# Optimization experiments

Measured on AMD Instinct MI355X. Metric: run time of the kernel, lower is better.

## Reference

```python
import jax, jax.numpy as jnp
import numpy as np


def setup_inputs() -> dict:
    key = jax.random.key(0)
    k1, k2 = jax.random.split(key)
    B, C, N = 8, 3, 4096
    ori_pcs = jax.random.normal(k1, (B, C, N), dtype=jnp.float32)
    adv_pcs = jax.random.normal(k2, (B, C, N), dtype=jnp.float32)
    return {"ori_pcs": ori_pcs, "adv_pcs": adv_pcs}


def _chamfer(ori_pcs, adv_pcs, single=False, reduce="max"):
    # [B, 3, N] -> [B, N, 3]
    x = jnp.swapaxes(ori_pcs, 1, 2)
    y = jnp.swapaxes(adv_pcs, 1, 2)
    x2 = jnp.sum(x * x, axis=-1)  # [B, N]
    y2 = jnp.sum(y * y, axis=-1)  # [B, M]
    # squared pairwise distances [B, N, M]
    d = x2[:, :, None] + y2[:, None, :] - 2.0 * jnp.einsum("bnd,bmd->bnm", x, y)
    d = jnp.maximum(d, 0.0)
    d1 = jnp.mean(jnp.min(d, axis=2), axis=1)  # ori -> adv, per batch [B]
    if single:
        return jnp.mean(d1)
    d2 = jnp.mean(jnp.min(d, axis=1), axis=1)  # adv -> ori, per batch [B]
    if reduce == "max":
        per_batch = jnp.maximum(d1, d2)
    else:  # 'sum' / 'mean' style fallback
        per_batch = d1 + d2
    return jnp.mean(per_batch)


def reference(ori_pcs, adv_pcs):
    return _chamfer(ori_pcs, adv_pcs, single=False, reduce="max")
```

## Files before the change

### kernel.cpp

```cpp
#include <hip/hip_runtime.h>
#include <float.h>

#define BATCH 8
#define NPTS 4096
#define BLK 256
#define THALF 1024
#define NH 4

typedef __attribute__((ext_vector_type(8))) short short8;
typedef __attribute__((ext_vector_type(16))) float floatx16;

union U4S8 { uint4 u; short8 s; };

__device__ inline unsigned short f2bf(float f) {
    unsigned u = __float_as_uint(f);
    return (unsigned short)((u + 0x7FFFu + ((u >> 16) & 1u)) >> 16);
}
__device__ inline float bf2f(unsigned short h) {
    return __uint_as_float(((unsigned)h) << 16);
}
__device__ inline unsigned flag_token(int i) {
    return 0x9E3779B9u * (unsigned)(i + 7);
}

__global__ __launch_bounds__(BLK, 4) void chamfer_partial(
        const float* __restrict__ ori, const float* __restrict__ adv,
        float* __restrict__ rfin) {
    __shared__ uint4 sm[THALF];

    int bx = blockIdx.x;
    int half = bx & (NH - 1);
    int rowgroup = (bx >> 2) & 15;
    int dirb = bx >> 6;
    int b = dirb & 7;
    int dir = dirb >> 3;

    const float* qsrc = dir ? adv : ori;
    const float* tsrc = dir ? ori : adv;

    {
        const float* tx = tsrc + (b * 3 + 0) * NPTS;
        const float* ty = tsrc + (b * 3 + 1) * NPTS;
        const float* tz = tsrc + (b * 3 + 2) * NPTS;
        #pragma unroll
        for (int i = 0; i < THALF / BLK; ++i) {
            int p = threadIdx.x + i * BLK;
            int m = half * THALF + p;
            float x = tx[m], y = ty[m], z = tz[m];
            float n2 = fmaf(x, x, fmaf(y, y, z * z));
            unsigned short hx = f2bf(x), hy = f2bf(y), hz = f2bf(z);
            unsigned short lx = f2bf(x - bf2f(hx));
            unsigned short ly = f2bf(y - bf2f(hy));
            unsigned short lz = f2bf(z - bf2f(hz));
            unsigned short h2 = f2bf(n2);
            unsigned short l2 = f2bf(n2 - bf2f(h2));
            uint4 u;
            u.x = (unsigned)hx | ((unsigned)hy << 16);
            u.y = (unsigned)hz | ((unsigned)lx << 16);
            u.z = (unsigned)ly | ((unsigned)lz << 16);
            u.w = (unsigned)h2 | ((unsigned)l2 << 16);
            sm[p] = u;
        }
    }

    int w = threadIdx.x >> 6;
    int l = threadIdx.x & 63;
    int lrow = l & 31;
    int kh = l >> 5;

    short8 afrag[2];
    #pragma unroll
    for (int bi = 0; bi < 2; ++bi) {
        int q = rowgroup * 256 + (w * 2 + bi) * 32 + lrow;
        float x = qsrc[(b * 3 + 0) * NPTS + q];
        float y = qsrc[(b * 3 + 1) * NPTS + q];
        float z = qsrc[(b * 3 + 2) * NPTS + q];
        float n2 = fmaf(x, x, fmaf(y, y, z * z));
        unsigned short hx = f2bf(x), hy = f2bf(y), hz = f2bf(z);
        unsigned short lx = f2bf(x - bf2f(hx));
        unsigned short ly = f2bf(y - bf2f(hy));
        unsigned short lz = f2bf(z - bf2f(hz));
        unsigned short h2 = f2bf(n2);
        unsigned short l2 = f2bf(n2 - bf2f(h2));
        unsigned short mhx = f2bf(-2.0f * bf2f(hx));
        unsigned short mhy = f2bf(-2.0f * bf2f(hy));
        unsigned short mhz = f2bf(-2.0f * bf2f(hz));
        unsigned short mlx = f2bf(-2.0f * bf2f(lx));
        unsigned short mly = f2bf(-2.0f * bf2f(ly));
        unsigned short mlz = f2bf(-2.0f * bf2f(lz));
        const unsigned short one = 0x3F80;
        union { unsigned short us[8]; short8 s8; } A;
        if (kh == 0) {
            A.us[0] = mhx; A.us[1] = mhy; A.us[2] = mhz;
            A.us[3] = mhx; A.us[4] = mhy; A.us[5] = mhz;
            A.us[6] = one; A.us[7] = one;
        } else {
            A.us[0] = mlx; A.us[1] = mly; A.us[2] = mlz;
            A.us[3] = h2;  A.us[4] = l2;
            A.us[5] = 0;   A.us[6] = 0;   A.us[7] = 0;
        }
        afrag[bi] = A.s8;
    }
    __syncthreads();

    floatx16 zero, rmn0, rmn1;
    #pragma unroll
    for (int r = 0; r < 16; ++r) { zero[r] = 0.0f; rmn0[r] = FLT_MAX; rmn1[r] = FLT_MAX; }

    bool hi = (kh == 1);
    int col = lrow;

#define PROCESS2(r0, r1)                                                       \
    {                                                                          \
        U4S8 f0, f1;                                                           \
        f0.u.x = (r0).x;                                                       \
        f0.u.y = hi ? (((r0).y & 0xFFFFu) | 0x3F800000u) : (r0).y;             \
        f0.u.z = hi ? 0x00003F80u : (r0).z;                                    \
        f0.u.w = hi ? 0u : (r0).w;                                             \
        f1.u.x = (r1).x;                                                       \
        f1.u.y = hi ? (((r1).y & 0xFFFFu) | 0x3F800000u) : (r1).y;             \
        f1.u.z = hi ? 0x00003F80u : (r1).z;                                    \
        f1.u.w = hi ? 0u : (r1).w;                                             \
        floatx16 a0 = __builtin_amdgcn_mfma_f32_32x32x16_bf16(afrag[0], f0.s, zero, 0, 0, 0); \
        floatx16 a1 = __builtin_amdgcn_mfma_f32_32x32x16_bf16(afrag[0], f1.s, zero, 0, 0, 0); \
        _Pragma("unroll")                                                      \
        for (int r = 0; r < 16; ++r)                                           \
            rmn0[r] = fminf(fminf(rmn0[r], a0[r]), a1[r]);                     \
        floatx16 c0 = __builtin_amdgcn_mfma_f32_32x32x16_bf16(afrag[1], f0.s, zero, 0, 0, 0); \
        floatx16 c1 = __builtin_amdgcn_mfma_f32_32x32x16_bf16(afrag[1], f1.s, zero, 0, 0, 0); \
        _Pragma("unroll")                                                      \
        for (int r = 0; r < 16; ++r)                                           \
            rmn1[r] = fminf(fminf(rmn1[r], c0[r]), c1[r]);                     \
    }

    {
        uint4 r0 = sm[col], r1 = sm[32 + col];
        #pragma unroll 1
        for (int ct = 0; ct < 30; ct += 2) {
            uint4 p0 = sm[(ct + 2) * 32 + col];
            uint4 p1 = sm[(ct + 3) * 32 + col];
            PROCESS2(r0, r1);
            r0 = p0; r1 = p1;
        }
        PROCESS2(r0, r1);
    }
#undef PROCESS2

    #pragma unroll
    for (int r = 0; r < 16; ++r) {
        float v0 = rmn0[r], v1 = rmn1[r];
        #pragma unroll
        for (int m = 1; m <= 16; m <<= 1) {
            v0 = fminf(v0, __shfl_xor(v0, m));
            v1 = fminf(v1, __shfl_xor(v1, m));
        }
        rmn0[r] = v0; rmn1[r] = v1;
    }
    if (lrow == 0) {
        float* base = rfin + (((size_t)(dirb * NH + half)) << 12)
                    + rowgroup * 256 + kh * 4;
        float* d0 = base + (w * 2 + 0) * 32;
        float* d1 = base + (w * 2 + 1) * 32;
        #pragma unroll
        for (int r = 0; r < 16; ++r) {
            int off = (r & 3) + 8 * (r >> 2);
            d0[off] = rmn0[r];
            d1[off] = rmn1[r];
        }
    }
}

__global__ __launch_bounds__(BLK) void combine_kernel(
        const float* __restrict__ rfin, float* __restrict__ bsum,
        unsigned* __restrict__ flags, float* __restrict__ out) {
    __shared__ float ws[4];
    __shared__ float sh[16];
    int dirb = blockIdx.x;
    const float* p = rfin + (((size_t)dirb * NH) << 12);
    float s = 0.0f;
    #pragma unroll
    for (int k = 0; k < 16; ++k) {
        int row = k * BLK + threadIdx.x;
        float m = fminf(fminf(p[row], p[(1 << 12) + row]),
                        fminf(p[(2 << 12) + row], p[(3 << 12) + row]));
        s += fmaxf(m, 0.0f);
    }
    for (int off = 32; off > 0; off >>= 1) s += __shfl_down(s, off);
    int wid = threadIdx.x >> 6, lane = threadIdx.x & 63;
    if (lane == 0) ws[wid] = s;
    __syncthreads();
    if (threadIdx.x == 0) {
        float t = ws[0] + ws[1] + ws[2] + ws[3];
        atomicExch((unsigned*)(bsum + dirb), __float_as_uint(t));
        __threadfence();
        atomicExch(flags + dirb, flag_token(dirb));
    }

    if (dirb == 0) {
        __syncthreads();
        int t = threadIdx.x;
        if (t < 16) {
            unsigned want = flag_token(t);
            while (atomicAdd(flags + t, 0u) != want) {
                __builtin_amdgcn_s_sleep(1);
            }
            sh[t] = __uint_as_float(atomicAdd((unsigned*)(bsum + t), 0u));
        }
        __syncthreads();
        if (t == 0) {
            float acc = 0.0f;
            #pragma unroll
            for (int bb = 0; bb < BATCH; ++bb)
                acc += fmaxf(sh[bb], sh[8 + bb]);
            out[0] = acc * (1.0f / (float)NPTS) * (1.0f / (float)BATCH);
        }
    }
}

extern "C" void kernel_launch(void* const* d_in, const int* in_sizes, int n_in,
                              void* d_out, int out_size, void* d_ws, size_t ws_size,
                              hipStream_t stream) {
    const float* ori = (const float*)d_in[0];
    const float* adv = (const float*)d_in[1];
    float* out = (float*)d_out;

    float* rfin = (float*)d_ws;
    float* bsum = rfin + (size_t)16 * NH * NPTS;
    unsigned* flags = (unsigned*)(bsum + 16);

    chamfer_partial<<<16 * 16 * NH, BLK, 0, stream>>>(ori, adv, rfin);
    combine_kernel<<<16, BLK, 0, stream>>>(rfin, bsum, flags, out);
}
```

Before: 23.26 us.

## Pre-build both B fragments in LDS and widen combine kernel to 256 blocks

The main kernel now writes two versions of each target point into shared memory, one per k-half of the MFMA B operand. The inner loop then loads the fragment directly, with no per-iteration select and mask ops. The combine kernel is split from 16 blocks into 256, each reducing one 256-row slice, and block 0 waits on 256 flags before a two-level final sum. This doubles LDS use per block and adds more spin-waiting in the final gather, in exchange for less VALU work in the hot loop and more parallel reduction.

```diff
diff --git a/kernel.cpp b/kernel.cpp
--- a/kernel.cpp
+++ b/kernel.cpp
@@ -26,7 +26,7 @@
 __global__ __launch_bounds__(BLK, 4) void chamfer_partial(
         const float* __restrict__ ori, const float* __restrict__ adv,
         float* __restrict__ rfin) {
-    __shared__ uint4 sm[THALF];
+    __shared__ uint4 fr[2 * THALF];
 
     int bx = blockIdx.x;
     int half = bx & (NH - 1);
@@ -54,12 +54,18 @@
             unsigned short lz = f2bf(z - bf2f(hz));
             unsigned short h2 = f2bf(n2);
             unsigned short l2 = f2bf(n2 - bf2f(h2));
-            uint4 u;
-            u.x = (unsigned)hx | ((unsigned)hy << 16);
-            u.y = (unsigned)hz | ((unsigned)lx << 16);
-            u.z = (unsigned)ly | ((unsigned)lz << 16);
-            u.w = (unsigned)h2 | ((unsigned)l2 << 16);
-            sm[p] = u;
+            uint4 v0;
+            v0.x = (unsigned)hx | ((unsigned)hy << 16);
+            v0.y = (unsigned)hz | ((unsigned)lx << 16);
+            v0.z = (unsigned)ly | ((unsigned)lz << 16);
+            v0.w = (unsigned)h2 | ((unsigned)l2 << 16);
+            uint4 v1;
+            v1.x = v0.x;
+            v1.y = (unsigned)hz | (0x3F80u << 16);
+            v1.z = 0x00003F80u;
+            v1.w = 0u;
+            fr[p] = v0;
+            fr[THALF + p] = v1;
         }
     }
 
@@ -107,20 +113,11 @@
     #pragma unroll
     for (int r = 0; r < 16; ++r) { zero[r] = 0.0f; rmn0[r] = FLT_MAX; rmn1[r] = FLT_MAX; }
 
-    bool hi = (kh == 1);
-    int col = lrow;
-
-#define PROCESS2(r0, r1)                                                       \
+    const uint4* tp = fr + kh * THALF + lrow;
+
+#define PROCESS2(f0u, f1u)                                                     \
     {                                                                          \
-        U4S8 f0, f1;                                                           \
-        f0.u.x = (r0).x;                                                       \
-        f0.u.y = hi ? (((r0).y & 0xFFFFu) | 0x3F800000u) : (r0).y;             \
-        f0.u.z = hi ? 0x00003F80u : (r0).z;                                    \
-        f0.u.w = hi ? 0u : (r0).w;                                             \
-        f1.u.x = (r1).x;                                                       \
-        f1.u.y = hi ? (((r1).y & 0xFFFFu) | 0x3F800000u) : (r1).y;             \
-        f1.u.z = hi ? 0x00003F80u : (r1).z;                                    \
-        f1.u.w = hi ? 0u : (r1).w;                                             \
+        U4S8 f0, f1; f0.u = (f0u); f1.u = (f1u);                               \
         floatx16 a0 = __builtin_amdgcn_mfma_f32_32x32x16_bf16(afrag[0], f0.s, zero, 0, 0, 0); \
         floatx16 a1 = __builtin_amdgcn_mfma_f32_32x32x16_bf16(afrag[0], f1.s, zero, 0, 0, 0); \
         _Pragma("unroll")                                                      \
@@ -134,11 +131,11 @@
     }
 
     {
-        uint4 r0 = sm[col], r1 = sm[32 + col];
+        uint4 r0 = tp[0], r1 = tp[32];
         #pragma unroll 1
         for (int ct = 0; ct < 30; ct += 2) {
-            uint4 p0 = sm[(ct + 2) * 32 + col];
-            uint4 p1 = sm[(ct + 3) * 32 + col];
+            uint4 p0 = tp[(ct + 2) * 32];
+            uint4 p1 = tp[(ct + 3) * 32];
             PROCESS2(r0, r1);
             r0 = p0; r1 = p1;
         }
@@ -171,47 +168,50 @@
 }
 
 __global__ __launch_bounds__(BLK) void combine_kernel(
-        const float* __restrict__ rfin, float* __restrict__ bsum,
+        const float* __restrict__ rfin, float* __restrict__ pb,
         unsigned* __restrict__ flags, float* __restrict__ out) {
     __shared__ float ws[4];
-    __shared__ float sh[16];
-    int dirb = blockIdx.x;
-    const float* p = rfin + (((size_t)dirb * NH) << 12);
-    float s = 0.0f;
-    #pragma unroll
-    for (int k = 0; k < 16; ++k) {
-        int row = k * BLK + threadIdx.x;
-        float m = fminf(fminf(p[row], p[(1 << 12) + row]),
-                        fminf(p[(2 << 12) + row], p[(3 << 12) + row]));
-        s += fmaxf(m, 0.0f);
-    }
+    __shared__ float sh[256 + 16];
+    int cb = blockIdx.x;
+    int dirb = cb >> 4;
+    int rs = cb & 15;
+    const float* p = rfin + (((size_t)dirb * NH) << 12) + rs * 256;
+    int row = threadIdx.x;
+    float m = fminf(fminf(p[row], p[(1 << 12) + row]),
+                    fminf(p[(2 << 12) + row], p[(3 << 12) + row]));
+    float s = fmaxf(m, 0.0f);
     for (int off = 32; off > 0; off >>= 1) s += __shfl_down(s, off);
     int wid = threadIdx.x >> 6, lane = threadIdx.x & 63;
     if (lane == 0) ws[wid] = s;
     __syncthreads();
     if (threadIdx.x == 0) {
         float t = ws[0] + ws[1] + ws[2] + ws[3];
-        atomicExch((unsigned*)(bsum + dirb), __float_as_uint(t));
+        atomicExch((unsigned*)(pb + cb), __float_as_uint(t));
         __threadfence();
-        atomicExch(flags + dirb, flag_token(dirb));
-    }
-
-    if (dirb == 0) {
+        atomicExch(flags + cb, flag_token(cb));
+    }
+
+    if (cb == 0) {
         __syncthreads();
         int t = threadIdx.x;
+        unsigned want = flag_token(t);
+        while (atomicAdd(flags + t, 0u) != want) {
+            __builtin_amdgcn_s_sleep(1);
+        }
+        sh[t] = __uint_as_float(atomicAdd((unsigned*)(pb + t), 0u));
+        __syncthreads();
         if (t < 16) {
-            unsigned want = flag_token(t);
-            while (atomicAdd(flags + t, 0u) != want) {
-                __builtin_amdgcn_s_sleep(1);
-            }
-            sh[t] = __uint_as_float(atomicAdd((unsigned*)(bsum + t), 0u));
+            float acc = 0.0f;
+            #pragma unroll
+            for (int c = 0; c < 16; ++c) acc += sh[t * 16 + c];
+            sh[256 + t] = acc;
         }
         __syncthreads();
         if (t == 0) {
             float acc = 0.0f;
             #pragma unroll
             for (int bb = 0; bb < BATCH; ++bb)
-                acc += fmaxf(sh[bb], sh[8 + bb]);
+                acc += fmaxf(sh[256 + bb], sh[256 + 8 + bb]);
             out[0] = acc * (1.0f / (float)NPTS) * (1.0f / (float)BATCH);
         }
     }
@@ -225,9 +225,9 @@
     float* out = (float*)d_out;
 
     float* rfin = (float*)d_ws;
-    float* bsum = rfin + (size_t)16 * NH * NPTS;
-    unsigned* flags = (unsigned*)(bsum + 16);
+    float* pb = rfin + (size_t)16 * NH * NPTS;
+    unsigned* flags = (unsigned*)(pb + 256);
 
     chamfer_partial<<<16 * 16 * NH, BLK, 0, stream>>>(ori, adv, rfin);
-    combine_kernel<<<16, BLK, 0, stream>>>(rfin, bsum, flags, out);
-}
+    combine_kernel<<<256, BLK, 0, stream>>>(rfin, pb, flags, out);
+}
```

New measurement: 25.55 us. 9.8% more time.

## Use 512-thread blocks with one query tile per wave

Applied to the files above, without the earlier changes.

Each block now has 8 waves instead of 4, and each wave handles a single 32-row query tile instead of two. The same 256 query rows per block are spread across more waves, so the target tile is staged into shared memory by more threads. Each wave holds half as many accumulators and issues half as many MFMAs per LDS read. This trades B-fragment reuse across two A fragments for more waves per CU, and each LDS read of target points now feeds fewer MFMAs. The launch bound of 4 blocks per CU is kept at the larger block size, which may constrain registers.

```diff
diff --git a/kernel.cpp b/kernel.cpp
--- a/kernel.cpp
+++ b/kernel.cpp
@@ -3,7 +3,7 @@
 
 #define BATCH 8
 #define NPTS 4096
-#define BLK 256
+#define BLK 512
 #define THALF 1024
 #define NH 4
 
@@ -68,10 +68,9 @@
     int lrow = l & 31;
     int kh = l >> 5;
 
-    short8 afrag[2];
-    #pragma unroll
-    for (int bi = 0; bi < 2; ++bi) {
-        int q = rowgroup * 256 + (w * 2 + bi) * 32 + lrow;
+    short8 afrag;
+    {
+        int q = rowgroup * 256 + w * 32 + lrow;
         float x = qsrc[(b * 3 + 0) * NPTS + q];
         float y = qsrc[(b * 3 + 1) * NPTS + q];
         float z = qsrc[(b * 3 + 2) * NPTS + q];
@@ -99,13 +98,13 @@
             A.us[3] = h2;  A.us[4] = l2;
             A.us[5] = 0;   A.us[6] = 0;   A.us[7] = 0;
         }
-        afrag[bi] = A.s8;
+        afrag = A.s8;
     }
     __syncthreads();
 
-    floatx16 zero, rmn0, rmn1;
+    floatx16 zero, rmn;
     #pragma unroll
-    for (int r = 0; r < 16; ++r) { zero[r] = 0.0f; rmn0[r] = FLT_MAX; rmn1[r] = FLT_MAX; }
+    for (int r = 0; r < 16; ++r) { zero[r] = 0.0f; rmn[r] = FLT_MAX; }
 
     bool hi = (kh == 1);
     int col = lrow;
@@ -121,16 +120,11 @@
         f1.u.y = hi ? (((r1).y & 0xFFFFu) | 0x3F800000u) : (r1).y;             \
         f1.u.z = hi ? 0x00003F80u : (r1).z;                                    \
         f1.u.w = hi ? 0u : (r1).w;                                             \
-        floatx16 a0 = __builtin_amdgcn_mfma_f32_32x32x16_bf16(afrag[0], f0.s, zero, 0, 0, 0); \
-        floatx16 a1 = __builtin_amdgcn_mfma_f32_32x32x16_bf16(afrag[0], f1.s, zero, 0, 0, 0); \
+        floatx16 a0 = __builtin_amdgcn_mfma_f32_32x32x16_bf16(afrag, f0.s, zero, 0, 0, 0); \
+        floatx16 a1 = __builtin_amdgcn_mfma_f32_32x32x16_bf16(afrag, f1.s, zero, 0, 0, 0); \
         _Pragma("unroll")                                                      \
         for (int r = 0; r < 16; ++r)                                           \
-            rmn0[r] = fminf(fminf(rmn0[r], a0[r]), a1[r]);                     \
-        floatx16 c0 = __builtin_amdgcn_mfma_f32_32x32x16_bf16(afrag[1], f0.s, zero, 0, 0, 0); \
-        floatx16 c1 = __builtin_amdgcn_mfma_f32_32x32x16_bf16(afrag[1], f1.s, zero, 0, 0, 0); \
-        _Pragma("unroll")                                                      \
-        for (int r = 0; r < 16; ++r)                                           \
-            rmn1[r] = fminf(fminf(rmn1[r], c0[r]), c1[r]);                     \
+            rmn[r] = fminf(fminf(rmn[r], a0[r]), a1[r]);        \
     }
 
     {
@@ -148,29 +142,22 @@
 
     #pragma unroll
     for (int r = 0; r < 16; ++r) {
-        float v0 = rmn0[r], v1 = rmn1[r];
+        float v = rmn[r];
         #pragma unroll
-        for (int m = 1; m <= 16; m <<= 1) {
-            v0 = fminf(v0, __shfl_xor(v0, m));
-            v1 = fminf(v1, __shfl_xor(v1, m));
-        }
-        rmn0[r] = v0; rmn1[r] = v1;
+        for (int m = 1; m <= 16; m <<= 1)
+            v = fminf(v, __shfl_xor(v, m));
+        rmn[r] = v;
     }
     if (lrow == 0) {
-        float* base = rfin + (((size_t)(dirb * NH + half)) << 12)
-                    + rowgroup * 256 + kh * 4;
-        float* d0 = base + (w * 2 + 0) * 32;
-        float* d1 = base + (w * 2 + 1) * 32;
+        float* d = rfin + (((size_t)(dirb * NH + half)) << 12)
+                 + rowgroup * 256 + w * 32 + kh * 4;
         #pragma unroll
-        for (int r = 0; r < 16; ++r) {
-            int off = (r & 3) + 8 * (r >> 2);
-            d0[off] = rmn0[r];
-            d1[off] = rmn1[r];
-        }
-    }
-}
-
-__global__ __launch_bounds__(BLK) void combine_kernel(
+        for (int r = 0; r < 16; ++r)
+            d[(r & 3) + 8 * (r >> 2)] = rmn[r];
+    }
+}
+
+__global__ __launch_bounds__(256) void combine_kernel(
         const float* __restrict__ rfin, float* __restrict__ bsum,
         unsigned* __restrict__ flags, float* __restrict__ out) {
     __shared__ float ws[4];
@@ -180,7 +167,7 @@
     float s = 0.0f;
     #pragma unroll
     for (int k = 0; k < 16; ++k) {
-        int row = k * BLK + threadIdx.x;
+        int row = k * 256 + threadIdx.x;
         float m = fminf(fminf(p[row], p[(1 << 12) + row]),
                         fminf(p[(2 << 12) + row], p[(3 << 12) + row]));
         s += fmaxf(m, 0.0f);
@@ -229,5 +216,5 @@
     unsigned* flags = (unsigned*)(bsum + 16);
 
     chamfer_partial<<<16 * 16 * NH, BLK, 0, stream>>>(ori, adv, rfin);
-    combine_kernel<<<16, BLK, 0, stream>>>(rfin, bsum, flags, out);
-}
+    combine_kernel<<<16, 256, 0, stream>>>(rfin, bsum, flags, out);
+}
```

Result: faster. 22.66 us (-2.6%).
